# Performance work log

Measured on AMD Instinct MI355X. Metric: run time of the kernel, lower is better.

Reference implementation:

```python
import jax, jax.numpy as jnp
import numpy as np

N, E, H = 50000, 800000, 4
IN, HID, OUT = 128, 64, 16
SIM_THRESH = 0.1
NEG_SLOPE = 0.01  # F.leaky_relu default


def setup_inputs() -> dict:
    key = jax.random.key(0)
    k = jax.random.split(key, 6)
    x = jax.random.normal(k[0], (N, IN), jnp.float32)
    row = jax.random.randint(k[1], (E,), 0, N)
    col = jax.random.randint(k[2], (E,), 0, N)
    W0 = jax.random.normal(k[3], (H, IN, HID), jnp.float32) / np.float32(np.sqrt(IN))
    W1 = jax.random.normal(k[4], (H, H * HID, HID), jnp.float32) / np.float32(np.sqrt(H * HID))
    W2 = jax.random.normal(k[5], (1, H * HID, OUT), jnp.float32) / np.float32(np.sqrt(H * HID))
    return {"x": x, "W0": W0, "W1": W1, "W2": W2, "row": row, "col": col}


def _att_coef(x, row, col):
    # cosine similarity on edges only (honors the sparse edge structure)
    nrm = jnp.linalg.norm(x, axis=1, keepdims=True)
    xn = x / jnp.maximum(nrm, 1e-12)
    sim = jnp.sum(xn[row] * xn[col], axis=1)            # [E]
    sim = jnp.where(sim < SIM_THRESH, 0.0, sim)
    # L1 row-normalize the thresholded attention matrix
    rowsum = jax.ops.segment_sum(jnp.abs(sim), row, num_segments=N)
    rs_e = rowsum[row]
    att = jnp.where(rs_e > 0, sim / jnp.where(rs_e > 0, rs_e, 1.0), 0.0)
    # degree-based self-loop weight lam = 1/(deg+1), then exp of all nonzeros
    deg = jax.ops.segment_sum((att != 0).astype(x.dtype), row, num_segments=N)
    w_edge = jnp.where(att != 0, jnp.exp(att), 0.0)     # zero entries stay zero (dropped nnz)
    w_self = jnp.exp(1.0 / (deg + 1.0))                 # [N]
    return w_edge, w_self


def _layer(x, W, row, col, act):
    w_edge, w_self = _att_coef(x, row, col)
    z = jnp.einsum('nd,hdo->nho', x, W)                 # per-head projection
    msg = w_edge[:, None, None] * z[col]                # [E,h,o] gather + weight
    agg = jax.ops.segment_sum(msg, row, num_segments=N) + w_self[:, None, None] * z
    out = agg.reshape(N, -1)                            # concat heads (flatten(1))
    return jax.nn.leaky_relu(out, NEG_SLOPE) if act else out


def reference(x, W0, W1, W2, row, col):
    h = _layer(x, W0, row, col, True)
    h = _layer(h, W1, row, col, True)
    h = _layer(h, W2, row, col, False)
    return h
```

## Files before the change

kernel.cpp:

```cpp
#include <hip/hip_runtime.h>
#include <math.h>


static inline int cdiv(int a, int b){ return (a + b - 1) / b; }


__device__ inline float vdot(float4 a, float4 b){ return a.x*b.x + a.y*b.y + a.z*b.z + a.w*b.w; }
__device__ inline void vfma(float4& acc, float w, float4 b){
  acc.x += w*b.x; acc.y += w*b.y; acc.z += w*b.z; acc.w += w*b.w;
}
__device__ inline float4 vscale(float w, float4 a){ return make_float4(w*a.x, w*a.y, w*a.z, w*a.w); }

__device__ inline float wred(float d){
  #pragma unroll
  for (int off = 32; off; off >>= 1) d += __shfl_xor(d, off);
  return d;
}

__device__ inline unsigned short f2bf(float f){
  unsigned int u = __float_as_uint(f);
  unsigned int r = (u + 0x7FFFu + ((u >> 16) & 1u)) >> 16;
  return (unsigned short)r;
}
__device__ inline float bf2f(unsigned int us){ return __uint_as_float(us << 16); }

__device__ inline void bf8_to_f(uint4 v, float* f){
  f[0] = bf2f(v.x & 0xFFFFu); f[1] = bf2f(v.x >> 16);
  f[2] = bf2f(v.y & 0xFFFFu); f[3] = bf2f(v.y >> 16);
  f[4] = bf2f(v.z & 0xFFFFu); f[5] = bf2f(v.z >> 16);
  f[6] = bf2f(v.w & 0xFFFFu); f[7] = bf2f(v.w >> 16);
}

typedef __attribute__((ext_vector_type(8))) short bf16x8;
typedef __attribute__((ext_vector_type(4))) float f32x4;


__global__ void count_kernel(const int* __restrict__ row, int* __restrict__ cnt, int E){
  int e = blockIdx.x * blockDim.x + threadIdx.x;
  if (e < E) atomicAdd(&cnt[row[e]], 1);
}

__global__ void scan1_kernel(const int* __restrict__ cnt, int* __restrict__ offs,
                             int* __restrict__ bsum, int n){
  __shared__ int tmp[256];
  int tid = threadIdx.x;
  int g = blockIdx.x * 256 + tid;
  int v = (g < n) ? cnt[g] : 0;
  tmp[tid] = v;
  __syncthreads();
  for (int off = 1; off < 256; off <<= 1){
    int t = (tid >= off) ? tmp[tid - off] : 0;
    __syncthreads();
    tmp[tid] += t;
    __syncthreads();
  }
  if (g < n) offs[g] = tmp[tid] - v;
  if (tid == 255) bsum[blockIdx.x] = tmp[255];
}

__global__ void scan2_kernel(int* __restrict__ bsum, int* __restrict__ offs, int nb, int n){
  __shared__ int tmp[256];
  int tid = threadIdx.x;
  int v = (tid < nb) ? bsum[tid] : 0;
  tmp[tid] = v;
  __syncthreads();
  for (int off = 1; off < 256; off <<= 1){
    int t = (tid >= off) ? tmp[tid - off] : 0;
    __syncthreads();
    tmp[tid] += t;
    __syncthreads();
  }
  if (tid < nb) bsum[tid] = tmp[tid] - v;
  if (tid == 255) offs[n] = tmp[255];
}

__global__ void scan3_kernel(int* __restrict__ offs, int* __restrict__ cur,
                             const int* __restrict__ bsum, int n){
  int g = blockIdx.x * 256 + threadIdx.x;
  if (g < n){
    int o = offs[g] + bsum[blockIdx.x];
    offs[g] = o;
    cur[g]  = o;
  }
}

__global__ void scatter_kernel(const int* __restrict__ row, const int* __restrict__ col,
                               int* __restrict__ cur, int* __restrict__ ecol, int E){
  int e = blockIdx.x * blockDim.x + threadIdx.x;
  if (e < E){
    int p = atomicAdd(&cur[row[e]], 1);
    ecol[p] = col[e];
  }
}


__global__ void invnorm128_kernel(const float* __restrict__ x, float* __restrict__ invn, int N){
  int n = blockIdx.x * 4 + (threadIdx.x >> 6);
  int lane = threadIdx.x & 63;
  if (n >= N) return;
  float2 a = ((const float2*)(x + (size_t)n * 128))[lane];
  float ss = a.x * a.x + a.y * a.y;
  ss = wred(ss);
  if (lane == 0) invn[n] = 1.0f / fmaxf(sqrtf(ss), 1e-12f);
}


template<int R>
__global__ void att_agg_wave128(const float* __restrict__ x, const float* __restrict__ invn,
                                const int* __restrict__ offs, const int* __restrict__ ecol,
                                float* __restrict__ out, int N){
  constexpr int LT = 64;
  __shared__ float tls[4][LT];
  __shared__ int   tlk[4][LT];
  const int wid  = threadIdx.x >> 6;
  const int lane = threadIdx.x & 63;
  const int half = lane >> 5, hl = lane & 31;
  const int hidx = wid * 2 + half;
  const int n = blockIdx.x * 2 + wid;
  if (n >= N) return;
  const int s = offs[n], e = offs[n + 1];
  const float inr = invn[n];
  const float4* xv = (const float4*)x;
  float4 a = xv[(size_t)n * 32 + hl];

  float4 br[R];
  float  simv[R];
  float  rowsum = 0.0f;
  int    deg = 0;

  #pragma unroll
  for (int r = 0; r < R; r++){
    simv[r] = 0.0f;
    int k = s + 2 * r + half;
    if (k < e){
      int c = ecol[k];
      float4 b = xv[(size_t)c * 32 + hl];
      br[r] = b;
      float d = vdot(a, b);
      #pragma unroll
      for (int off = 16; off; off >>= 1) d += __shfl_xor(d, off);
      d *= inr * invn[c];
      if (d < 0.1f) d = 0.0f;
      simv[r] = d;
      rowsum += d;
      deg += (d != 0.0f) ? 1 : 0;
    }
  }

  int tc = 0, kover = e;
  int k = s + 2 * R + half;
  for (; k + 2 < e; k += 4){
    int c0 = ecol[k], c1 = ecol[k + 2];
    float4 b0 = xv[(size_t)c0 * 32 + hl];
    float4 b1 = xv[(size_t)c1 * 32 + hl];
    float d0 = vdot(a, b0), d1 = vdot(a, b1);
    #pragma unroll
    for (int off = 16; off; off >>= 1){ d0 += __shfl_xor(d0, off); d1 += __shfl_xor(d1, off); }
    d0 *= inr * invn[c0];
    d1 *= inr * invn[c1];
    if (d0 < 0.1f) d0 = 0.0f;
    if (d1 < 0.1f) d1 = 0.0f;
    rowsum += d0 + d1;
    deg += (d0 != 0.0f) + (d1 != 0.0f);
    if (d0 > 0.0f){
      if (tc < LT){ if (hl == 0){ tls[hidx][tc] = d0; tlk[hidx][tc] = c0; } tc++; }
      else if (kover > k) kover = k;
    }
    if (d1 > 0.0f){
      if (tc < LT){ if (hl == 0){ tls[hidx][tc] = d1; tlk[hidx][tc] = c1; } tc++; }
      else if (kover > k + 2) kover = k + 2;
    }
  }
  if (k < e){
    int c0 = ecol[k];
    float4 b0 = xv[(size_t)c0 * 32 + hl];
    float d0 = vdot(a, b0);
    #pragma unroll
    for (int off = 16; off; off >>= 1) d0 += __shfl_xor(d0, off);
    d0 *= inr * invn[c0];
    if (d0 < 0.1f) d0 = 0.0f;
    rowsum += d0;
    deg += (d0 != 0.0f) ? 1 : 0;
    if (d0 > 0.0f){
      if (tc < LT){ if (hl == 0){ tls[hidx][tc] = d0; tlk[hidx][tc] = c0; } tc++; }
      else if (kover > k) kover = k;
    }
  }

  rowsum += __shfl_xor(rowsum, 32);
  deg    += __shfl_xor(deg, 32);
  const float invrs = (rowsum > 0.0f) ? 1.0f / rowsum : 0.0f;
  const float wself = expf(1.0f / (float)(deg + 1));

  float4 acc = (half == 0) ? vscale(wself, a) : make_float4(0.f, 0.f, 0.f, 0.f);
  #pragma unroll
  for (int r = 0; r < R; r++){
    if (simv[r] > 0.0f) vfma(acc, expf(simv[r] * invrs), br[r]);
  }
  int j = 0;
  for (; j + 1 < tc; j += 2){
    float w0 = expf(tls[hidx][j] * invrs);
    float w1 = expf(tls[hidx][j + 1] * invrs);
    int c0 = tlk[hidx][j], c1 = tlk[hidx][j + 1];
    float4 b0 = xv[(size_t)c0 * 32 + hl];
    float4 b1 = xv[(size_t)c1 * 32 + hl];
    vfma(acc, w0, b0);
    vfma(acc, w1, b1);
  }
  if (j < tc){
    float w0 = expf(tls[hidx][j] * invrs);
    float4 b0 = xv[(size_t)tlk[hidx][j] * 32 + hl];
    vfma(acc, w0, b0);
  }
  for (int k2 = kover; k2 < e; k2 += 2){
    int c = ecol[k2];
    float4 b = xv[(size_t)c * 32 + hl];
    float d = vdot(a, b);
    #pragma unroll
    for (int off = 16; off; off >>= 1) d += __shfl_xor(d, off);
    d *= inr * invn[c];
    if (d >= 0.1f) vfma(acc, expf(d * invrs), b);
  }

  acc.x += __shfl_xor(acc.x, 32);
  acc.y += __shfl_xor(acc.y, 32);
  acc.z += __shfl_xor(acc.z, 32);
  acc.w += __shfl_xor(acc.w, 32);
  if (half == 0) ((float4*)out)[(size_t)n * 32 + hl] = acc;
}


template<int LT>
__device__ inline void sim_rows_mfma(const uint4* __restrict__ hb4,
                                     const float* __restrict__ invn,
                                     const int* __restrict__ ecol,
                                     int n, int s, int e, float inr,
                                     float* __restrict__ tls, int* __restrict__ tlk,
                                     float& rowsum_o, int& deg_o, int& tcl_o, int& kover_o){
  const int l = threadIdx.x & 63;
  const int g = l >> 4;
  const bf16x8* hbv = (const bf16x8*)hb4;

  bf16x8 bfrag[8];
  #pragma unroll
  for (int f = 0; f < 8; f++) bfrag[f] = hbv[(size_t)n * 32 + f * 4 + g];

  float rowsum = 0.0f;
  int deg = 0, tc = 0, kover = e;

  for (int k0 = s; k0 < e; k0 += 16){
    int idx = k0 + (l & 15);
    int kk = (idx < e) ? idx : (e - 1);
    int c_l = ecol[kk];
    float ic_l = invn[c_l];
    const size_t cb = (size_t)c_l * 32 + g;
    f32x4 acc0 = {0.f, 0.f, 0.f, 0.f};
    f32x4 acc1 = {0.f, 0.f, 0.f, 0.f};
    #pragma unroll
    for (int f = 0; f < 8; f += 2){
      bf16x8 av0 = hbv[cb + (size_t)f * 4];
      bf16x8 av1 = hbv[cb + (size_t)(f + 1) * 4];
      acc0 = __builtin_amdgcn_mfma_f32_16x16x32_bf16(av0, bfrag[f],     acc0, 0, 0, 0);
      acc1 = __builtin_amdgcn_mfma_f32_16x16x32_bf16(av1, bfrag[f + 1], acc1, 0, 0, 0);
    }
    float dv[4]; int cm[4];
    int bits = 0;
    #pragma unroll
    for (int r = 0; r < 4; r++){
      int m = g * 4 + r;
      cm[r] = __shfl(c_l, m);
      float ic = __shfl(ic_l, m);
      float d = (acc0[r] + acc1[r]) * inr * ic;
      if (d < 0.1f || (k0 + m) >= e) d = 0.0f;
      dv[r] = d;
      rowsum += d;
      deg += (d != 0.0f) ? 1 : 0;
      if (d > 0.0f) bits |= (1 << r);
    }
    int M16 = bits << (g * 4);
    M16 |= __shfl_xor(M16, 16);
    M16 |= __shfl_xor(M16, 32);
    #pragma unroll
    for (int r = 0; r < 4; r++){
      if ((l & 15) == 0 && dv[r] > 0.0f){
        int m = g * 4 + r;
        int pos = tc + __popc(M16 & ((1 << m) - 1));
        if (pos < LT){ tls[pos] = dv[r]; tlk[pos] = cm[r]; }
        else if (k0 + m < kover) kover = k0 + m;
      }
    }
    tc += __popc(M16);
  }
  rowsum += __shfl_xor(rowsum, 16);
  rowsum += __shfl_xor(rowsum, 32);
  deg    += __shfl_xor(deg, 16);
  deg    += __shfl_xor(deg, 32);
  #pragma unroll
  for (int off = 32; off; off >>= 1) kover = min(kover, __shfl_xor(kover, off));
  rowsum_o = rowsum; deg_o = deg;
  tcl_o = (tc < LT) ? tc : LT;
  kover_o = kover;
}


template<int LT>
__global__ __launch_bounds__(128) void att256_mfma(
    const unsigned short* __restrict__ hbf, const float* __restrict__ invn,
    const int* __restrict__ offs, const int* __restrict__ ecol,
    float* __restrict__ out, int N){
  __shared__ float tls[2][LT];
  __shared__ int   tlk[2][LT];
  const int wid = threadIdx.x >> 6;
  const int l   = threadIdx.x & 63;
  const int n = blockIdx.x * 2 + wid;
  if (n >= N) return;
  const int s = offs[n], e = offs[n + 1];
  const float inr = invn[n];
  const uint4* hb4 = (const uint4*)hbf;

  float rowsum; int deg, tcl, kover;
  sim_rows_mfma<LT>(hb4, invn, ecol, n, s, e, inr, tls[wid], tlk[wid],
                    rowsum, deg, tcl, kover);

  const float invrs = (rowsum > 0.0f) ? 1.0f / rowsum : 0.0f;
  const float wself = expf(1.0f / (float)(deg + 1));

  const int half = l >> 5, hl = l & 31;
  float a8[8]; bf8_to_f(hb4[(size_t)n * 32 + hl], a8);
  float acc8[8];
  #pragma unroll
  for (int t = 0; t < 8; t++) acc8[t] = (half == 0) ? wself * a8[t] : 0.0f;

  int j = half;
  for (; j + 2 < tcl; j += 4){
    float w0 = expf(tls[wid][j] * invrs);
    float w1 = expf(tls[wid][j + 2] * invrs);
    uint4 v0 = hb4[(size_t)tlk[wid][j] * 32 + hl];
    uint4 v1 = hb4[(size_t)tlk[wid][j + 2] * 32 + hl];
    float b0[8], b1[8];
    bf8_to_f(v0, b0); bf8_to_f(v1, b1);
    #pragma unroll
    for (int t = 0; t < 8; t++) acc8[t] += w0 * b0[t] + w1 * b1[t];
  }
  if (j < tcl){
    float w0 = expf(tls[wid][j] * invrs);
    uint4 v0 = hb4[(size_t)tlk[wid][j] * 32 + hl];
    float b0[8]; bf8_to_f(v0, b0);
    #pragma unroll
    for (int t = 0; t < 8; t++) acc8[t] += w0 * b0[t];
  }
  for (int k2 = kover; k2 < e; k2++){
    int c = ecol[k2];
    uint4 v = hb4[(size_t)c * 32 + hl];
    float b[8]; bf8_to_f(v, b);
    float d = 0.0f;
    #pragma unroll
    for (int t = 0; t < 8; t++) d += a8[t] * b[t];
    #pragma unroll
    for (int off = 16; off; off >>= 1) d += __shfl_xor(d, off);
    d *= inr * invn[c];
    if (d >= 0.1f && half == 0){
      float w = expf(d * invrs);
      #pragma unroll
      for (int t = 0; t < 8; t++) acc8[t] += w * b[t];
    }
  }

  #pragma unroll
  for (int t = 0; t < 8; t++) acc8[t] += __shfl_xor(acc8[t], 32);
  if (half == 0){
    float4* ov = (float4*)out;
    ov[(size_t)n * 64 + 2 * hl]     = make_float4(acc8[0], acc8[1], acc8[2], acc8[3]);
    ov[(size_t)n * 64 + 2 * hl + 1] = make_float4(acc8[4], acc8[5], acc8[6], acc8[7]);
  }
}


template<int LT>
__global__ __launch_bounds__(128) void attz16_mfma(
    const unsigned short* __restrict__ hbf, const float* __restrict__ invn,
    const int* __restrict__ offs, const int* __restrict__ ecol,
    const float* __restrict__ z2, float* __restrict__ out, int N){
  __shared__ float tls[2][LT];
  __shared__ int   tlk[2][LT];
  const int wid = threadIdx.x >> 6;
  const int l   = threadIdx.x & 63;
  const int n = blockIdx.x * 2 + wid;
  if (n >= N) return;
  const int s = offs[n], e = offs[n + 1];
  const float inr = invn[n];
  const uint4* hb4 = (const uint4*)hbf;

  float rowsum; int deg, tcl, kover;
  sim_rows_mfma<LT>(hb4, invn, ecol, n, s, e, inr, tls[wid], tlk[wid],
                    rowsum, deg, tcl, kover);

  const float invrs = (rowsum > 0.0f) ? 1.0f / rowsum : 0.0f;
  const float wself = expf(1.0f / (float)(deg + 1));

  const int g = l >> 4, ch = l & 15;
  float acc = 0.0f;
  for (int j = g; j < tcl; j += 4){
    float w = expf(tls[wid][j] * invrs);
    acc += w * z2[(size_t)tlk[wid][j] * 16 + ch];
  }
  if (kover < e){
    const int hl = l & 31;
    float a8[8]; bf8_to_f(hb4[(size_t)n * 32 + hl], a8);
    for (int k2 = kover; k2 < e; k2++){
      int c = ecol[k2];
      uint4 v = hb4[(size_t)c * 32 + hl];
      float b[8]; bf8_to_f(v, b);
      float d = 0.0f;
      #pragma unroll
      for (int t = 0; t < 8; t++) d += a8[t] * b[t];
      #pragma unroll
      for (int off = 16; off; off >>= 1) d += __shfl_xor(d, off);
      d *= inr * invn[c];
      if (d >= 0.1f && g == 0)
        acc += expf(d * invrs) * z2[(size_t)c * 16 + ch];
    }
  }
  acc += __shfl_xor(acc, 16);
  acc += __shfl_xor(acc, 32);
  if (l < 16) out[(size_t)n * 16 + l] = acc + wself * z2[(size_t)n * 16 + l];
}


template<int D>
__global__ __launch_bounds__(256) void proj_act_norm(
    const float* __restrict__ xin, const float* __restrict__ W,
    float* __restrict__ hout, float* __restrict__ invn,
    unsigned short* __restrict__ hbf, int N){
  __shared__ float xs[32][D];
  const int tid = threadIdx.x;
  const int w = tid >> 6, l = tid & 63;
  const int n0 = blockIdx.x * 32;

  {
    float4* xs4 = (float4*)&xs[0][0];
    const float4* xin4 = (const float4*)(xin + (size_t)n0 * D);
    const int rows = (N - n0 >= 32) ? 32 : (N - n0);
    const int limit4 = rows * (D / 4);
    constexpr int total4 = 32 * D / 4;
    for (int i = tid; i < total4; i += 256)
      xs4[i] = (i < limit4) ? xin4[i] : make_float4(0.f, 0.f, 0.f, 0.f);
  }
  __syncthreads();

  const int h  = l >> 4;
  const int oo = (l & 15) * 4;
  const float* Wp = W + (size_t)h * D * 64 + oo;
  const float* xrow = &xs[w * 8][0];

  float acc[8][4];
  #pragma unroll
  for (int i = 0; i < 8; i++){
    acc[i][0] = 0.f; acc[i][1] = 0.f; acc[i][2] = 0.f; acc[i][3] = 0.f;
  }

  for (int d = 0; d < D; d += 4){
    float4 w0 = *(const float4*)(Wp + (size_t)(d + 0) * 64);
    float4 w1 = *(const float4*)(Wp + (size_t)(d + 1) * 64);
    float4 w2 = *(const float4*)(Wp + (size_t)(d + 2) * 64);
    float4 w3 = *(const float4*)(Wp + (size_t)(d + 3) * 64);
    #pragma unroll
    for (int i = 0; i < 8; i++){
      float4 xv = *(const float4*)(xrow + i * D + d);
      acc[i][0] += xv.x * w0.x + xv.y * w1.x + xv.z * w2.x + xv.w * w3.x;
      acc[i][1] += xv.x * w0.y + xv.y * w1.y + xv.z * w2.y + xv.w * w3.y;
      acc[i][2] += xv.x * w0.z + xv.y * w1.z + xv.z * w2.z + xv.w * w3.z;
      acc[i][3] += xv.x * w0.w + xv.y * w1.w + xv.z * w2.w + xv.w * w3.w;
    }
  }

  const int nrow = n0 + w * 8;
  #pragma unroll
  for (int i = 0; i < 8; i++){
    #pragma unroll
    for (int j = 0; j < 4; j++){
      float a = acc[i][j];
      acc[i][j] = (a > 0.0f) ? a : 0.01f * a;
    }
    float ss = acc[i][0]*acc[i][0] + acc[i][1]*acc[i][1]
             + acc[i][2]*acc[i][2] + acc[i][3]*acc[i][3];
    ss = wred(ss);
    const int n = nrow + i;
    if (n < N){
      if (l == 0) invn[n] = 1.0f / fmaxf(sqrtf(ss), 1e-12f);
      ((float4*)hout)[(size_t)n * 64 + l] =
          make_float4(acc[i][0], acc[i][1], acc[i][2], acc[i][3]);
      if (hbf){
        ushort4 u;
        u.x = f2bf(acc[i][0]); u.y = f2bf(acc[i][1]);
        u.z = f2bf(acc[i][2]); u.w = f2bf(acc[i][3]);
        ((ushort4*)hbf)[(size_t)n * 64 + l] = u;
      }
    }
  }
}

__global__ void proj16_kernel(const float* __restrict__ x, const float* __restrict__ W,
                              float* __restrict__ z, int N){
  __shared__ float xs[16][256];
  __shared__ float wsh[256 * 16];
  int tid = threadIdx.x;
  int n0 = blockIdx.x * 16;
  for (int i = tid; i < 16 * 256; i += 256){
    int nl = i >> 8, d = i & 255;
    int n = n0 + nl;
    xs[nl][d] = (n < N) ? x[(size_t)n * 256 + d] : 0.0f;
  }
  for (int i = tid; i < 256 * 16; i += 256) wsh[i] = W[i];
  __syncthreads();
  int nl = tid >> 4, o = tid & 15;
  float acc = 0.0f;
  for (int d = 0; d < 256; d++) acc += xs[nl][d] * wsh[d * 16 + o];
  int n = n0 + nl;
  if (n < N) z[(size_t)n * 16 + o] = acc;
}


extern "C" void kernel_launch(void* const* d_in, const int* in_sizes, int n_in,
                              void* d_out, int out_size, void* d_ws, size_t ws_size,
                              hipStream_t stream){
  const float* x  = (const float*)d_in[0];
  const float* W0 = (const float*)d_in[1];
  const float* W1 = (const float*)d_in[2];
  const float* W2 = (const float*)d_in[3];
  const int*   row = (const int*)d_in[4];
  const int*   col = (const int*)d_in[5];
  const int N = in_sizes[0] / 128;
  const int E = in_sizes[4];
  float* out = (float*)d_out;

  float* p = (float*)d_ws;
  float* hbuf   = p; p += (size_t)N * 256;
  float* aggbuf = p; p += (size_t)N * 256;
  float* z2     = p; p += (size_t)N * 16;
  float* invn   = p; p += N;
  unsigned short* hbf = (unsigned short*)p; p += (size_t)N * 128;
  int* cnt  = (int*)p;
  int* offs = cnt + N;
  int* cur  = offs + N + 1;
  int* ecol = cur + N;
  int* bsum = ecol + E;

  const int NB = cdiv(N, 256);

  hipMemsetAsync(cnt, 0, sizeof(int) * N, stream);
  count_kernel<<<cdiv(E, 256), 256, 0, stream>>>(row, cnt, E);
  scan1_kernel<<<NB, 256, 0, stream>>>(cnt, offs, bsum, N);
  scan2_kernel<<<1, 256, 0, stream>>>(bsum, offs, NB, N);
  scan3_kernel<<<NB, 256, 0, stream>>>(offs, cur, bsum, N);
  scatter_kernel<<<cdiv(E, 256), 256, 0, stream>>>(row, col, cur, ecol, E);

  invnorm128_kernel<<<cdiv(N, 4), 256, 0, stream>>>(x, invn, N);
  att_agg_wave128<8><<<cdiv(N, 2), 128, 0, stream>>>(x, invn, offs, ecol, aggbuf, N);
  proj_act_norm<128><<<cdiv(N, 32), 256, 0, stream>>>(aggbuf, W0, hbuf, invn, hbf, N);

  att256_mfma<256><<<cdiv(N, 2), 128, 0, stream>>>(hbf, invn, offs, ecol, aggbuf, N);
  proj_act_norm<256><<<cdiv(N, 32), 256, 0, stream>>>(aggbuf, W1, hbuf, invn, hbf, N);

  proj16_kernel<<<cdiv(N, 16), 256, 0, stream>>>(hbuf, W2, z2, N);
  attz16_mfma<256><<<cdiv(N, 2), 128, 0, stream>>>(hbf, invn, offs, ecol, z2, out, N);
}
```

Measured before the change: 690.9 us.

## Convert attention kernels to persistent grid-stride loops with smaller LDS tiles

```diff
diff --git a/kernel.cpp b/kernel.cpp
--- a/kernel.cpp
+++ b/kernel.cpp
@@ -106,9 +106,10 @@
 
 
 template<int R>
-__global__ void att_agg_wave128(const float* __restrict__ x, const float* __restrict__ invn,
-                                const int* __restrict__ offs, const int* __restrict__ ecol,
-                                float* __restrict__ out, int N){
+__global__ __launch_bounds__(128) void att_agg_wave128(
+    const float* __restrict__ x, const float* __restrict__ invn,
+    const int* __restrict__ offs, const int* __restrict__ ecol,
+    float* __restrict__ out, int N){
   constexpr int LT = 64;
   __shared__ float tls[4][LT];
   __shared__ int   tlk[4][LT];
@@ -116,11 +117,12 @@
   const int lane = threadIdx.x & 63;
   const int half = lane >> 5, hl = lane & 31;
   const int hidx = wid * 2 + half;
-  const int n = blockIdx.x * 2 + wid;
-  if (n >= N) return;
+  const int nstride = gridDim.x * 2;
+  const float4* xv = (const float4*)x;
+
+  for (int n = blockIdx.x * 2 + wid; n < N; n += nstride){
   const int s = offs[n], e = offs[n + 1];
   const float inr = invn[n];
-  const float4* xv = (const float4*)x;
   float4 a = xv[(size_t)n * 32 + hl];
 
   float4 br[R];
@@ -227,6 +229,7 @@
   acc.z += __shfl_xor(acc.z, 32);
   acc.w += __shfl_xor(acc.w, 32);
   if (half == 0) ((float4*)out)[(size_t)n * 32 + hl] = acc;
+  }
 }
 
 
@@ -235,15 +238,12 @@
                                      const float* __restrict__ invn,
                                      const int* __restrict__ ecol,
                                      int n, int s, int e, float inr,
+                                     const bf16x8 (&bfrag)[8],
                                      float* __restrict__ tls, int* __restrict__ tlk,
                                      float& rowsum_o, int& deg_o, int& tcl_o, int& kover_o){
   const int l = threadIdx.x & 63;
   const int g = l >> 4;
   const bf16x8* hbv = (const bf16x8*)hb4;
-
-  bf16x8 bfrag[8];
-  #pragma unroll
-  for (int f = 0; f < 8; f++) bfrag[f] = hbv[(size_t)n * 32 + f * 4 + g];
 
   float rowsum = 0.0f;
   int deg = 0, tc = 0, kover = e;
@@ -312,26 +312,48 @@
   __shared__ int   tlk[2][LT];
   const int wid = threadIdx.x >> 6;
   const int l   = threadIdx.x & 63;
-  const int n = blockIdx.x * 2 + wid;
-  if (n >= N) return;
+  const int g = l >> 4;
+  const int half = l >> 5, hl = l & 31;
+  const int nstride = gridDim.x * 2;
+  const uint4* hb4 = (const uint4*)hbf;
+  const bf16x8* hbv = (const bf16x8*)hbf;
+
+  for (int n = blockIdx.x * 2 + wid; n < N; n += nstride){
   const int s = offs[n], e = offs[n + 1];
   const float inr = invn[n];
-  const uint4* hb4 = (const uint4*)hbf;
+
+  bf16x8 bfrag[8];
+  #pragma unroll
+  for (int f = 0; f < 8; f++) bfrag[f] = hbv[(size_t)n * 32 + f * 4 + g];
 
   float rowsum; int deg, tcl, kover;
-  sim_rows_mfma<LT>(hb4, invn, ecol, n, s, e, inr, tls[wid], tlk[wid],
+  sim_rows_mfma<LT>(hb4, invn, ecol, n, s, e, inr, bfrag, tls[wid], tlk[wid],
                     rowsum, deg, tcl, kover);
 
   const float invrs = (rowsum > 0.0f) ? 1.0f / rowsum : 0.0f;
   const float wself = expf(1.0f / (float)(deg + 1));
 
-  const int half = l >> 5, hl = l & 31;
   float a8[8]; bf8_to_f(hb4[(size_t)n * 32 + hl], a8);
   float acc8[8];
   #pragma unroll
   for (int t = 0; t < 8; t++) acc8[t] = (half == 0) ? wself * a8[t] : 0.0f;
 
   int j = half;
+  for (; j + 6 < tcl; j += 8){
+    float w0 = expf(tls[wid][j] * invrs);
+    float w1 = expf(tls[wid][j + 2] * invrs);
+    float w2 = expf(tls[wid][j + 4] * invrs);
+    float w3 = expf(tls[wid][j + 6] * invrs);
+    uint4 v0 = hb4[(size_t)tlk[wid][j] * 32 + hl];
+    uint4 v1 = hb4[(size_t)tlk[wid][j + 2] * 32 + hl];
+    uint4 v2 = hb4[(size_t)tlk[wid][j + 4] * 32 + hl];
+    uint4 v3 = hb4[(size_t)tlk[wid][j + 6] * 32 + hl];
+    float b0[8], b1[8], b2[8], b3[8];
+    bf8_to_f(v0, b0); bf8_to_f(v1, b1); bf8_to_f(v2, b2); bf8_to_f(v3, b3);
+    #pragma unroll
+    for (int t = 0; t < 8; t++)
+      acc8[t] += w0 * b0[t] + w1 * b1[t] + w2 * b2[t] + w3 * b3[t];
+  }
   for (; j + 2 < tcl; j += 4){
     float w0 = expf(tls[wid][j] * invrs);
     float w1 = expf(tls[wid][j + 2] * invrs);
@@ -372,6 +394,7 @@
     float4* ov = (float4*)out;
     ov[(size_t)n * 64 + 2 * hl]     = make_float4(acc8[0], acc8[1], acc8[2], acc8[3]);
     ov[(size_t)n * 64 + 2 * hl + 1] = make_float4(acc8[4], acc8[5], acc8[6], acc8[7]);
+  }
   }
 }
 
@@ -385,20 +408,27 @@
   __shared__ int   tlk[2][LT];
   const int wid = threadIdx.x >> 6;
   const int l   = threadIdx.x & 63;
-  const int n = blockIdx.x * 2 + wid;
-  if (n >= N) return;
+  const int g = l >> 4;
+  const int nstride = gridDim.x * 2;
+  const uint4* hb4 = (const uint4*)hbf;
+  const bf16x8* hbv = (const bf16x8*)hbf;
+
+  for (int n = blockIdx.x * 2 + wid; n < N; n += nstride){
   const int s = offs[n], e = offs[n + 1];
   const float inr = invn[n];
-  const uint4* hb4 = (const uint4*)hbf;
+
+  bf16x8 bfrag[8];
+  #pragma unroll
+  for (int f = 0; f < 8; f++) bfrag[f] = hbv[(size_t)n * 32 + f * 4 + g];
 
   float rowsum; int deg, tcl, kover;
-  sim_rows_mfma<LT>(hb4, invn, ecol, n, s, e, inr, tls[wid], tlk[wid],
+  sim_rows_mfma<LT>(hb4, invn, ecol, n, s, e, inr, bfrag, tls[wid], tlk[wid],
                     rowsum, deg, tcl, kover);
 
   const float invrs = (rowsum > 0.0f) ? 1.0f / rowsum : 0.0f;
   const float wself = expf(1.0f / (float)(deg + 1));
 
-  const int g = l >> 4, ch = l & 15;
+  const int ch = l & 15;
   float acc = 0.0f;
   for (int j = g; j < tcl; j += 4){
     float w = expf(tls[wid][j] * invrs);
@@ -424,6 +454,7 @@
   acc += __shfl_xor(acc, 16);
   acc += __shfl_xor(acc, 32);
   if (l < 16) out[(size_t)n * 16 + l] = acc + wself * z2[(size_t)n * 16 + l];
+  }
 }
 
 
@@ -547,6 +578,7 @@
   int* bsum = ecol + E;
 
   const int NB = cdiv(N, 256);
+  const int PG = 4096;
 
   hipMemsetAsync(cnt, 0, sizeof(int) * N, stream);
   count_kernel<<<cdiv(E, 256), 256, 0, stream>>>(row, cnt, E);
@@ -556,12 +588,12 @@
   scatter_kernel<<<cdiv(E, 256), 256, 0, stream>>>(row, col, cur, ecol, E);
 
   invnorm128_kernel<<<cdiv(N, 4), 256, 0, stream>>>(x, invn, N);
-  att_agg_wave128<8><<<cdiv(N, 2), 128, 0, stream>>>(x, invn, offs, ecol, aggbuf, N);
+  att_agg_wave128<8><<<PG, 128, 0, stream>>>(x, invn, offs, ecol, aggbuf, N);
   proj_act_norm<128><<<cdiv(N, 32), 256, 0, stream>>>(aggbuf, W0, hbuf, invn, hbf, N);
 
-  att256_mfma<256><<<cdiv(N, 2), 128, 0, stream>>>(hbf, invn, offs, ecol, aggbuf, N);
+  att256_mfma<128><<<PG, 128, 0, stream>>>(hbf, invn, offs, ecol, aggbuf, N);
   proj_act_norm<256><<<cdiv(N, 32), 256, 0, stream>>>(aggbuf, W1, hbuf, invn, hbf, N);
 
   proj16_kernel<<<cdiv(N, 16), 256, 0, stream>>>(hbuf, W2, z2, N);
-  attz16_mfma<256><<<cdiv(N, 2), 128, 0, stream>>>(hbf, invn, offs, ecol, z2, out, N);
-}
+  attz16_mfma<128><<<PG, 128, 0, stream>>>(hbf, invn, offs, ecol, z2, out, N);
+}
```

Result: slower. 733.2 us (+6.1%).
